# Kernel optimization log

Hardware: AMD Instinct MI355X
Metric: run time of the kernel (lower is better)

The kernel has to match this reference:

```python
import jax, jax.numpy as jnp
import numpy as np

EPS = 1e-07

def setup_inputs() -> dict:
    key = jax.random.key(0)
    k1, k2, k3, k4 = jax.random.split(key, 4)
    B, C, H, W = 16, 512, 64, 64
    NC = 256
    P = 2048
    feat = jax.random.normal(k1, (B, C, H, W), dtype=jnp.float32)
    patch_id = jax.random.randint(k2, (P,), 0, H * W, dtype=jnp.int64)
    # init_weights 'normal' with gain 0.02: N(0, 0.02) weights, zero biases
    w1 = jax.random.normal(k3, (NC, C), dtype=jnp.float32) * 0.02
    b1 = jnp.zeros((NC,), dtype=jnp.float32)
    w2 = jax.random.normal(k4, (NC, NC), dtype=jnp.float32) * 0.02
    b2 = jnp.zeros((NC,), dtype=jnp.float32)
    return {"feat": feat, "patch_id": patch_id, "w1": w1, "b1": b1, "w2": w2, "b2": b2}

def reference(feat, patch_id, w1, b1, w2, b2):
    B, C, H, W = feat.shape
    # [B, C, H, W] -> [B, H*W, C]
    feat_reshape = jnp.transpose(feat, (0, 2, 3, 1)).reshape(B, H * W, C)
    # gather sampled patches: [B, P, C] -> [B*P, C]
    x = feat_reshape[:, patch_id, :].reshape(-1, C)
    # 2-layer MLP (torch Linear: x @ W.T + b)
    h = jax.nn.relu(x @ w1.T + b1)
    y = h @ w2.T + b2
    # L2 normalize over feature dim (power=2)
    norm = jnp.sqrt(jnp.sum(y * y, axis=1, keepdims=True))
    return y / (norm + EPS)
```

## Files before the change

kernel.cpp:

```cpp
#include <hip/hip_runtime.h>
#include <hip/hip_bf16.h>

typedef __bf16 bf16x8 __attribute__((ext_vector_type(8)));
typedef __bf16 bf16x4 __attribute__((ext_vector_type(4)));
typedef float  f32x4  __attribute__((ext_vector_type(4)));

constexpr int Bn  = 16;
constexpr int Cc  = 512;
constexpr int HWn = 4096;
constexpr int Pn  = 2048;
constexpr int NC  = 256;
constexpr int Mdense = Bn * HWn;
constexpr int Mout   = Bn * Pn;
constexpr int BM   = 128;
constexpr int NTHR = 512;

__device__ __forceinline__ int swz(int row, int byte_in_row) {
  return row * 128 + (byte_in_row ^ ((row & 7) << 4));
}

__device__ __forceinline__ f32x4 mfma16(bf16x8 a, bf16x8 b, f32x4 c) {
  return __builtin_amdgcn_mfma_f32_16x16x32_bf16(a, b, c, 0, 0, 0);
}

__global__ __launch_bounds__(NTHR, 4)
void k1_dense(const float* __restrict__ feat, const float* __restrict__ w1,
              const float* __restrict__ b1, __bf16* __restrict__ h) {
  __shared__ __align__(16) char sB[NC * 128];

  const int tid = threadIdx.x;
  const int m0  = blockIdx.x * BM;
  const int b   = m0 >> 12;
  const int hw0 = m0 & (HWn - 1);
  const int wid = tid >> 6, lane = tid & 63;
  const int wm = wid >> 1, wn = wid & 1;
  const int g = lane >> 4, ln = lane & 15;

  f32x4 acc[2][8];
  #pragma unroll
  for (int rt = 0; rt < 2; ++rt)
    #pragma unroll
    for (int ct = 0; ct < 8; ++ct) acc[rt][ct] = (f32x4){0.f, 0.f, 0.f, 0.f};

  const float* gA0 = feat + (((size_t)(b * Cc + g * 8)) << 12) + hw0 + wm * 32 + ln;
  const float* gA1 = gA0 + 16;

  for (int kt = 0; kt < Cc / 64; ++kt) {
    bf16x8 af[2][2];
    const float* p0 = gA0 + (((size_t)(kt * 64)) << 12);
    const float* p1 = gA1 + (((size_t)(kt * 64)) << 12);
    #pragma unroll
    for (int ki = 0; ki < 2; ++ki)
      #pragma unroll
      for (int j = 0; j < 8; ++j) {
        af[0][ki][j] = (__bf16)p0[((size_t)(ki * 32 + j)) << 12];
        af[1][ki][j] = (__bf16)p1[((size_t)(ki * 32 + j)) << 12];
      }
    #pragma unroll
    for (int r = 0; r < 8; ++r) {
      int idx = tid + r * NTHR;
      int n = idx >> 4, kq = idx & 15;
      float4 f = *(const float4*)(w1 + (size_t)n * Cc + kt * 64 + kq * 4);
      bf16x4 v; v[0] = (__bf16)f.x; v[1] = (__bf16)f.y; v[2] = (__bf16)f.z; v[3] = (__bf16)f.w;
      *(uint2*)(sB + swz(n, kq * 8)) = __builtin_bit_cast(uint2, v);
    }
    __syncthreads();
    #pragma unroll
    for (int ki = 0; ki < 2; ++ki)
      #pragma unroll
      for (int ct = 0; ct < 8; ++ct) {
        bf16x8 bv = *(const bf16x8*)(sB + swz(wn * 128 + ct * 16 + ln, ki * 64 + g * 16));
        acc[0][ct] = mfma16(af[0][ki], bv, acc[0][ct]);
        acc[1][ct] = mfma16(af[1][ki], bv, acc[1][ct]);
      }
    __syncthreads();
  }

  #pragma unroll
  for (int ct = 0; ct < 8; ++ct) {
    const int col = wn * 128 + ct * 16 + ln;
    const float bias = b1[col];
    #pragma unroll
    for (int rt = 0; rt < 2; ++rt)
      #pragma unroll
      for (int j = 0; j < 4; ++j) {
        int row = m0 + wm * 32 + rt * 16 + g * 4 + j;
        float v = acc[rt][ct][j] + bias;
        h[(size_t)row * NC + col] = (__bf16)(v > 0.f ? v : 0.f);
      }
  }
}

__global__ __launch_bounds__(NTHR, 2)
void k2_gather(const __bf16* __restrict__ h, const int* __restrict__ pid,
               const float* __restrict__ w2, const float* __restrict__ b2,
               float* __restrict__ out) {
  __shared__ __align__(16) char sA[BM * 128];
  __shared__ __align__(16) char sB[NC * 128];
  __shared__ int sRow[BM];
  __shared__ float sRS[BM][2];

  const int tid = threadIdx.x;
  const int m0  = blockIdx.x * BM;
  const int img = m0 >> 11;
  const int p0  = m0 & (Pn - 1);
  if (tid < BM) sRow[tid] = img * HWn + pid[p0 + tid];
  __syncthreads();

  const int wid = tid >> 6, lane = tid & 63;
  const int wm = wid >> 1, wn = wid & 1;
  const int g = lane >> 4, ln = lane & 15;

  f32x4 acc[2][8];
  #pragma unroll
  for (int rt = 0; rt < 2; ++rt)
    #pragma unroll
    for (int ct = 0; ct < 8; ++ct) acc[rt][ct] = (f32x4){0.f, 0.f, 0.f, 0.f};

  const char* hb = (const char*)h;
  for (int kt = 0; kt < NC / 64; ++kt) {
    #pragma unroll
    for (int r = 0; r < 2; ++r) {
      int idx = tid + r * NTHR;
      int mm = idx >> 3, c8 = idx & 7;
      uint4 v = *(const uint4*)(hb + (size_t)sRow[mm] * 512 + kt * 128 + c8 * 16);
      *(uint4*)(sA + swz(mm, c8 * 16)) = v;
    }
    #pragma unroll
    for (int r = 0; r < 8; ++r) {
      int idx = tid + r * NTHR;
      int n = idx >> 4, kq = idx & 15;
      float4 f = *(const float4*)(w2 + (size_t)n * NC + kt * 64 + kq * 4);
      bf16x4 v; v[0] = (__bf16)f.x; v[1] = (__bf16)f.y; v[2] = (__bf16)f.z; v[3] = (__bf16)f.w;
      *(uint2*)(sB + swz(n, kq * 8)) = __builtin_bit_cast(uint2, v);
    }
    __syncthreads();
    #pragma unroll
    for (int ki = 0; ki < 2; ++ki) {
      bf16x8 a0 = *(const bf16x8*)(sA + swz(wm * 32 + ln,      ki * 64 + g * 16));
      bf16x8 a1 = *(const bf16x8*)(sA + swz(wm * 32 + 16 + ln, ki * 64 + g * 16));
      #pragma unroll
      for (int ct = 0; ct < 8; ++ct) {
        bf16x8 bv = *(const bf16x8*)(sB + swz(wn * 128 + ct * 16 + ln, ki * 64 + g * 16));
        acc[0][ct] = mfma16(a0, bv, acc[0][ct]);
        acc[1][ct] = mfma16(a1, bv, acc[1][ct]);
      }
    }
    __syncthreads();
  }

  float ss[2][4] = {{0.f,0.f,0.f,0.f},{0.f,0.f,0.f,0.f}};
  #pragma unroll
  for (int ct = 0; ct < 8; ++ct) {
    const int col = wn * 128 + ct * 16 + ln;
    const float bias = b2[col];
    #pragma unroll
    for (int rt = 0; rt < 2; ++rt)
      #pragma unroll
      for (int j = 0; j < 4; ++j) {
        float v = acc[rt][ct][j] + bias;
        acc[rt][ct][j] = v;
        ss[rt][j] += v * v;
      }
  }
  #pragma unroll
  for (int mk = 1; mk < 16; mk <<= 1)
    #pragma unroll
    for (int rt = 0; rt < 2; ++rt)
      #pragma unroll
      for (int j = 0; j < 4; ++j)
        ss[rt][j] += __shfl_xor(ss[rt][j], mk);
  if (ln == 0) {
    #pragma unroll
    for (int rt = 0; rt < 2; ++rt)
      #pragma unroll
      for (int j = 0; j < 4; ++j)
        sRS[wm * 32 + rt * 16 + g * 4 + j][wn] = ss[rt][j];
  }
  __syncthreads();
  float sc[2][4];
  #pragma unroll
  for (int rt = 0; rt < 2; ++rt)
    #pragma unroll
    for (int j = 0; j < 4; ++j) {
      int row = wm * 32 + rt * 16 + g * 4 + j;
      float t = sRS[row][0] + sRS[row][1];
      sc[rt][j] = 1.f / (sqrtf(t) + 1e-7f);
    }
  #pragma unroll
  for (int ct = 0; ct < 8; ++ct) {
    const int col = wn * 128 + ct * 16 + ln;
    #pragma unroll
    for (int rt = 0; rt < 2; ++rt)
      #pragma unroll
      for (int j = 0; j < 4; ++j) {
        int row = wm * 32 + rt * 16 + g * 4 + j;
        out[(size_t)(m0 + row) * NC + col] = acc[rt][ct][j] * sc[rt][j];
      }
  }
}

extern "C" void kernel_launch(void* const* d_in, const int* in_sizes, int n_in,
                              void* d_out, int out_size, void* d_ws, size_t ws_size,
                              hipStream_t stream) {
  const float* feat = (const float*)d_in[0];
  const int*   pid  = (const int*)d_in[1];
  const float* w1   = (const float*)d_in[2];
  const float* b1   = (const float*)d_in[3];
  const float* w2   = (const float*)d_in[4];
  const float* b2   = (const float*)d_in[5];
  float*  out  = (float*)d_out;
  __bf16* hbuf = (__bf16*)d_ws;

  k1_dense <<<Mdense / BM, NTHR, 0, stream>>>(feat, w1, b1, hbuf);
  k2_gather<<<Mout   / BM, NTHR, 0, stream>>>(hbuf, pid, w2, b2, out);
}
```

Baseline: 264.6 us.

## Pre-convert weights to bf16 and register-prefetch next K tile in both GEMMs

```diff
diff --git a/kernel.cpp b/kernel.cpp
--- a/kernel.cpp
+++ b/kernel.cpp
@@ -5,74 +5,91 @@
 typedef __bf16 bf16x4 __attribute__((ext_vector_type(4)));
 typedef float  f32x4  __attribute__((ext_vector_type(4)));
 
-constexpr int Bn  = 16;
 constexpr int Cc  = 512;
 constexpr int HWn = 4096;
 constexpr int Pn  = 2048;
 constexpr int NC  = 256;
-constexpr int Mdense = Bn * HWn;
-constexpr int Mout   = Bn * Pn;
+constexpr int Mdense = 16 * HWn;
+constexpr int Mout   = 16 * Pn;
 constexpr int BM   = 128;
 constexpr int NTHR = 512;
 
 __device__ __forceinline__ int swz(int row, int byte_in_row) {
   return row * 128 + (byte_in_row ^ ((row & 7) << 4));
 }
-
 __device__ __forceinline__ f32x4 mfma16(bf16x8 a, bf16x8 b, f32x4 c) {
   return __builtin_amdgcn_mfma_f32_16x16x32_bf16(a, b, c, 0, 0, 0);
 }
 
+__global__ void k0_prep(const float* __restrict__ w1, const float* __restrict__ w2,
+                        __bf16* __restrict__ w1b, __bf16* __restrict__ w2b) {
+  int i = blockIdx.x * 256 + threadIdx.x;
+  const float4 f = (i < 32768) ? ((const float4*)w1)[i] : ((const float4*)w2)[i - 32768];
+  bf16x4 v; v[0] = (__bf16)f.x; v[1] = (__bf16)f.y; v[2] = (__bf16)f.z; v[3] = (__bf16)f.w;
+  if (i < 32768) ((bf16x4*)w1b)[i] = v;
+  else           ((bf16x4*)w2b)[i - 32768] = v;
+}
+
 __global__ __launch_bounds__(NTHR, 4)
-void k1_dense(const float* __restrict__ feat, const float* __restrict__ w1,
+void k1_dense(const float* __restrict__ feat, const __bf16* __restrict__ w1b,
               const float* __restrict__ b1, __bf16* __restrict__ h) {
+  __shared__ __align__(16) char sA[BM * 128];
   __shared__ __align__(16) char sB[NC * 128];
 
   const int tid = threadIdx.x;
   const int m0  = blockIdx.x * BM;
-  const int b   = m0 >> 12;
-  const int hw0 = m0 & (HWn - 1);
+  const int b   = m0 >> 12, hw0 = m0 & (HWn - 1);
   const int wid = tid >> 6, lane = tid & 63;
   const int wm = wid >> 1, wn = wid & 1;
   const int g = lane >> 4, ln = lane & 15;
 
+  const int c0 = (tid & 15) * 4, p40 = tid >> 4;
+  const float* aBase = feat + (((size_t)(b * Cc + c0)) << 12) + hw0 + p40 * 4;
+  const int nB = tid >> 3, c8 = tid & 7;
+  const __bf16* bBase = w1b + (size_t)nB * Cc + c8 * 8;
+
   f32x4 acc[2][8];
   #pragma unroll
   for (int rt = 0; rt < 2; ++rt)
     #pragma unroll
     for (int ct = 0; ct < 8; ++ct) acc[rt][ct] = (f32x4){0.f, 0.f, 0.f, 0.f};
 
-  const float* gA0 = feat + (((size_t)(b * Cc + g * 8)) << 12) + hw0 + wm * 32 + ln;
-  const float* gA1 = gA0 + 16;
+  f32x4 pA[4]; uint4 pB[4];
+  #pragma unroll
+  for (int r = 0; r < 4; ++r) pA[r] = *(const f32x4*)(aBase + (((size_t)r) << 12));
+  #pragma unroll
+  for (int r = 0; r < 4; ++r) pB[r] = *(const uint4*)(bBase + (size_t)(64 * r) * Cc);
 
   for (int kt = 0; kt < Cc / 64; ++kt) {
-    bf16x8 af[2][2];
-    const float* p0 = gA0 + (((size_t)(kt * 64)) << 12);
-    const float* p1 = gA1 + (((size_t)(kt * 64)) << 12);
-    #pragma unroll
-    for (int ki = 0; ki < 2; ++ki)
-      #pragma unroll
-      for (int j = 0; j < 8; ++j) {
-        af[0][ki][j] = (__bf16)p0[((size_t)(ki * 32 + j)) << 12];
-        af[1][ki][j] = (__bf16)p1[((size_t)(ki * 32 + j)) << 12];
-      }
-    #pragma unroll
-    for (int r = 0; r < 8; ++r) {
-      int idx = tid + r * NTHR;
-      int n = idx >> 4, kq = idx & 15;
-      float4 f = *(const float4*)(w1 + (size_t)n * Cc + kt * 64 + kq * 4);
-      bf16x4 v; v[0] = (__bf16)f.x; v[1] = (__bf16)f.y; v[2] = (__bf16)f.z; v[3] = (__bf16)f.w;
-      *(uint2*)(sB + swz(n, kq * 8)) = __builtin_bit_cast(uint2, v);
-    }
-    __syncthreads();
-    #pragma unroll
-    for (int ki = 0; ki < 2; ++ki)
+    #pragma unroll
+    for (int i = 0; i < 4; ++i) {
+      bf16x4 v; v[0] = (__bf16)pA[0][i]; v[1] = (__bf16)pA[1][i];
+                v[2] = (__bf16)pA[2][i]; v[3] = (__bf16)pA[3][i];
+      *(uint2*)(sA + swz(p40 * 4 + i, c0 * 2)) = __builtin_bit_cast(uint2, v);
+    }
+    #pragma unroll
+    for (int r = 0; r < 4; ++r)
+      *(uint4*)(sB + swz(nB + 64 * r, c8 * 16)) = pB[r];
+    __syncthreads();
+    if (kt < Cc / 64 - 1) {
+      const float*  a2 = aBase + (((size_t)((kt + 1) * 64)) << 12);
+      const __bf16* b2 = bBase + (kt + 1) * 64;
+      #pragma unroll
+      for (int r = 0; r < 4; ++r) pA[r] = *(const f32x4*)(a2 + (((size_t)r) << 12));
+      #pragma unroll
+      for (int r = 0; r < 4; ++r) pB[r] = *(const uint4*)(b2 + (size_t)(64 * r) * Cc);
+    }
+    #pragma unroll
+    for (int ki = 0; ki < 2; ++ki) {
+      bf16x8 a0 = *(const bf16x8*)(sA + swz(wm * 32 + ln,      ki * 64 + g * 16));
+      bf16x8 a1 = *(const bf16x8*)(sA + swz(wm * 32 + 16 + ln, ki * 64 + g * 16));
       #pragma unroll
       for (int ct = 0; ct < 8; ++ct) {
         bf16x8 bv = *(const bf16x8*)(sB + swz(wn * 128 + ct * 16 + ln, ki * 64 + g * 16));
-        acc[0][ct] = mfma16(af[0][ki], bv, acc[0][ct]);
-        acc[1][ct] = mfma16(af[1][ki], bv, acc[1][ct]);
-      }
+        acc[0][ct] = mfma16(a0, bv, acc[0][ct]);
+        acc[1][ct] = mfma16(a1, bv, acc[1][ct]);
+      }
+    }
     __syncthreads();
   }
 
@@ -91,9 +108,9 @@
   }
 }
 
-__global__ __launch_bounds__(NTHR, 2)
+__global__ __launch_bounds__(NTHR, 4)
 void k2_gather(const __bf16* __restrict__ h, const int* __restrict__ pid,
-               const float* __restrict__ w2, const float* __restrict__ b2,
+               const __bf16* __restrict__ w2b, const float* __restrict__ b2,
                float* __restrict__ out) {
   __shared__ __align__(16) char sA[BM * 128];
   __shared__ __align__(16) char sB[NC * 128];
@@ -111,30 +128,40 @@
   const int wm = wid >> 1, wn = wid & 1;
   const int g = lane >> 4, ln = lane & 15;
 
+  const int mmA = tid >> 3, c8 = tid & 7;
+  const int nB = mmA;
+  const __bf16* bBase = w2b + (size_t)nB * NC + c8 * 8;
+  const char* hb = (const char*)h;
+
   f32x4 acc[2][8];
   #pragma unroll
   for (int rt = 0; rt < 2; ++rt)
     #pragma unroll
     for (int ct = 0; ct < 8; ++ct) acc[rt][ct] = (f32x4){0.f, 0.f, 0.f, 0.f};
 
-  const char* hb = (const char*)h;
+  uint4 qA[2], qB[4];
+  #pragma unroll
+  for (int r = 0; r < 2; ++r)
+    qA[r] = *(const uint4*)(hb + (size_t)sRow[mmA + 64 * r] * 512 + c8 * 16);
+  #pragma unroll
+  for (int r = 0; r < 4; ++r) qB[r] = *(const uint4*)(bBase + (size_t)(64 * r) * NC);
+
   for (int kt = 0; kt < NC / 64; ++kt) {
     #pragma unroll
-    for (int r = 0; r < 2; ++r) {
-      int idx = tid + r * NTHR;
-      int mm = idx >> 3, c8 = idx & 7;
-      uint4 v = *(const uint4*)(hb + (size_t)sRow[mm] * 512 + kt * 128 + c8 * 16);
-      *(uint4*)(sA + swz(mm, c8 * 16)) = v;
-    }
-    #pragma unroll
-    for (int r = 0; r < 8; ++r) {
-      int idx = tid + r * NTHR;
-      int n = idx >> 4, kq = idx & 15;
-      float4 f = *(const float4*)(w2 + (size_t)n * NC + kt * 64 + kq * 4);
-      bf16x4 v; v[0] = (__bf16)f.x; v[1] = (__bf16)f.y; v[2] = (__bf16)f.z; v[3] = (__bf16)f.w;
-      *(uint2*)(sB + swz(n, kq * 8)) = __builtin_bit_cast(uint2, v);
-    }
-    __syncthreads();
+    for (int r = 0; r < 2; ++r)
+      *(uint4*)(sA + swz(mmA + 64 * r, c8 * 16)) = qA[r];
+    #pragma unroll
+    for (int r = 0; r < 4; ++r)
+      *(uint4*)(sB + swz(nB + 64 * r, c8 * 16)) = qB[r];
+    __syncthreads();
+    if (kt < NC / 64 - 1) {
+      #pragma unroll
+      for (int r = 0; r < 2; ++r)
+        qA[r] = *(const uint4*)(hb + (size_t)sRow[mmA + 64 * r] * 512 + (kt + 1) * 128 + c8 * 16);
+      const __bf16* b2p = bBase + (kt + 1) * 64;
+      #pragma unroll
+      for (int r = 0; r < 4; ++r) qB[r] = *(const uint4*)(b2p + (size_t)(64 * r) * NC);
+    }
     #pragma unroll
     for (int ki = 0; ki < 2; ++ki) {
       bf16x8 a0 = *(const bf16x8*)(sA + swz(wm * 32 + ln,      ki * 64 + g * 16));
@@ -209,9 +236,14 @@
   const float* b1   = (const float*)d_in[3];
   const float* w2   = (const float*)d_in[4];
   const float* b2   = (const float*)d_in[5];
-  float*  out  = (float*)d_out;
-  __bf16* hbuf = (__bf16*)d_ws;
-
-  k1_dense <<<Mdense / BM, NTHR, 0, stream>>>(feat, w1, b1, hbuf);
-  k2_gather<<<Mout   / BM, NTHR, 0, stream>>>(hbuf, pid, w2, b2, out);
-}
+  float* out = (float*)d_out;
+
+  char* ws = (char*)d_ws;
+  __bf16* w1b = (__bf16*)ws;
+  __bf16* w2b = (__bf16*)(ws + 262144);
+  __bf16* hbuf = (__bf16*)(ws + (1 << 20));
+
+  k0_prep <<<192, 256, 0, stream>>>(w1, w2, w1b, w2b);
+  k1_dense<<<Mdense / BM, NTHR, 0, stream>>>(feat, w1b, b1, hbuf);
+  k2_gather<<<Mout / BM, NTHR, 0, stream>>>(hbuf, pid, w2b, b2, out);
+}
```

New measurement: 270.3 us. +2.1%, slower.
